# Kernel tuning notes

Measured on AMD Instinct MI355X. Metric: run time of the kernel, lower is better.

The kernel has to match this reference:

```python
import jax, jax.numpy as jnp
import numpy as np

EPS = 1e-6
NUM_GROUPS = 16


def group_norm(x, gamma, beta):
    # x: [B, C, H, W]
    B, C, H, W = x.shape
    xg = x.reshape(B, NUM_GROUPS, C // NUM_GROUPS, H, W)
    mean = xg.mean(axis=(2, 3, 4), keepdims=True)
    var = xg.var(axis=(2, 3, 4), keepdims=True)
    xg = (xg - mean) * jax.lax.rsqrt(var + EPS)
    x = xg.reshape(B, C, H, W)
    return x * gamma[None, :, None, None] + beta[None, :, None, None]


def conv1x1(x, w, b):
    # x: [B, C, H, W], w: [O, C], b: [O]
    return jnp.einsum('bchw,oc->bohw', x, w) + b[None, :, None, None]


def setup_inputs() -> dict:
    key = jax.random.key(0)
    ks = jax.random.split(key, 6)
    B, C, H, W = 8, 256, 64, 64
    s = 1.0 / np.sqrt(C)
    return {
        'x': jax.random.normal(ks[0], (B, C, H, W), dtype=jnp.float32),
        'gamma': jnp.ones((C,), jnp.float32),
        'beta': jnp.zeros((C,), jnp.float32),
        'wq': jax.random.normal(ks[1], (C, C), dtype=jnp.float32) * s,
        'bq': jnp.zeros((C,), jnp.float32),
        'wk': jax.random.normal(ks[2], (C, C), dtype=jnp.float32) * s,
        'bk': jnp.zeros((C,), jnp.float32),
        'wv': jax.random.normal(ks[3], (C, C), dtype=jnp.float32) * s,
        'bv': jnp.zeros((C,), jnp.float32),
        'wp': jax.random.normal(ks[4], (C, C), dtype=jnp.float32) * s,
        'bp': jnp.zeros((C,), jnp.float32),
    }


def reference(x, gamma, beta, wq, bq, wk, bk, wv, bv, wp, bp):
    B, C, H, W = x.shape
    identity = x
    h = group_norm(x, gamma, beta)
    q = conv1x1(h, wq, bq).reshape(B, C, H * W)  # [B, C, N]
    k = conv1x1(h, wk, bk).reshape(B, C, H * W)
    v = conv1x1(h, wv, bv).reshape(B, C, H * W)
    # alpha[b, i, j] = sum_c q[b, c, i] * k[b, c, j], scaled by C^-0.5
    alpha = jnp.einsum('bci,bcj->bij', q, k) * (C ** -0.5)
    alpha = jax.nn.softmax(alpha, axis=-1)
    # out[b, c, i] = sum_j v[b, c, j] * alpha[b, i, j]
    out = jnp.einsum('bcj,bij->bci', v, alpha).reshape(B, C, H, W)
    out = conv1x1(out, wp, bp)
    return identity + out
```

## Files before the change

kernel.cpp:

```cpp
#include <hip/hip_runtime.h>
#include <hip/hip_bf16.h>


typedef unsigned int u32;
typedef unsigned short u16;
typedef __bf16 bf16x8 __attribute__((ext_vector_type(8)));
typedef float f32x4 __attribute__((ext_vector_type(4)));
typedef float f32x16 __attribute__((ext_vector_type(16)));

#define GAS __attribute__((address_space(1)))
#define LAS __attribute__((address_space(3)))

__device__ __forceinline__ u16 f2bf(float f) {
  union { float f; u32 u; } v; v.f = f;
  return (u16)((v.u + 0x7fffu + ((v.u >> 16) & 1u)) >> 16);
}

__device__ __forceinline__ f32x16 mfma32(bf16x8 a, bf16x8 b, f32x16 c) {
  return __builtin_amdgcn_mfma_f32_32x32x16_bf16(a, b, c, 0, 0, 0);
}

template<int ITERS, int NT>
__device__ __forceinline__ void stage_lin(u16* lds, const u16* g, int tid) {
#pragma unroll
  for (int it = 0; it < ITERS; ++it) {
    int idx = it * NT + tid;
    const u16* src = g + (long)idx * 8;
    u16* dst = lds + (long)(idx & ~63) * 8;
    __builtin_amdgcn_global_load_lds((const GAS u32*)src, (LAS u32*)dst, 16, 0, 0);
  }
}

template<int ROWS, int NT>
__device__ __forceinline__ void stage_gran(u16* lds, const u16* g, int k0, int tid) {
  constexpr int ITERS = 4 * ROWS / NT;
#pragma unroll
  for (int it = 0; it < ITERS; ++it) {
    int gi = it * NT + tid;
    int row = gi & (ROWS - 1);
    int kh = gi / ROWS;
    const u16* src = g + (long)row * 256 + k0 + kh * 8;
    u16* dst = lds + (long)(gi & ~63) * 8;
    __builtin_amdgcn_global_load_lds((const GAS u32*)src, (LAS u32*)dst, 16, 0, 0);
  }
}

__global__ __launch_bounds__(256) void convert_w(
    const float* __restrict__ w0, const float* __restrict__ w1,
    const float* __restrict__ w2, const float* __restrict__ w3,
    u16* __restrict__ out) {
  int i = blockIdx.x * 256 + threadIdx.x;
  int seg = i >> 16, idx = i & 65535;
  const float* w = seg == 0 ? w0 : seg == 1 ? w1 : seg == 2 ? w2 : w3;
  out[i] = f2bf(w[idx]);
}

__global__ __launch_bounds__(256) void gn_kernel(
    const float* __restrict__ x, const float* __restrict__ gamma,
    const float* __restrict__ beta, u16* __restrict__ ht) {
  int tid = threadIdx.x;
  int b = blockIdx.x >> 4;
  int grp = blockIdx.x & 15;
  const float* xg = x + ((long)b * 256 + grp * 16) * 4096;

  float s = 0.f, ss = 0.f;
  const float4* x4 = (const float4*)xg;
#pragma unroll 4
  for (int it = 0; it < 64; ++it) {
    float4 v = x4[it * 256 + tid];
    s += v.x + v.y + v.z + v.w;
    ss += v.x * v.x + v.y * v.y + v.z * v.z + v.w * v.w;
  }
#pragma unroll
  for (int d = 1; d < 64; d <<= 1) {
    s += __shfl_xor(s, d);
    ss += __shfl_xor(ss, d);
  }
  __shared__ float red[10];
  int lane = tid & 63, wave = tid >> 6;
  if (lane == 0) { red[wave] = s; red[4 + wave] = ss; }
  __syncthreads();
  if (tid == 0) {
    float S = red[0] + red[1] + red[2] + red[3];
    float SS = red[4] + red[5] + red[6] + red[7];
    float mean = S * (1.f / 65536.f);
    float var = SS * (1.f / 65536.f) - mean * mean;
    red[8] = mean;
    red[9] = rsqrtf(var + 1e-6f);
  }
  __syncthreads();
  float mean = red[8], rstd = red[9];

  float a[16], bb[16];
#pragma unroll
  for (int c = 0; c < 16; ++c) {
    float gm = gamma[grp * 16 + c];
    float bt = beta[grp * 16 + c];
    a[c] = gm * rstd;
    bb[c] = bt - mean * a[c];
  }
  u16* hb = ht + (long)b * 4096 * 256 + grp * 16;
  for (int it = 0; it < 16; ++it) {
    int n = it * 256 + tid;
    __align__(16) u16 tmp[16];
#pragma unroll
    for (int c = 0; c < 16; ++c)
      tmp[c] = f2bf(xg[(long)c * 4096 + n] * a[c] + bb[c]);
    u16* dst = hb + (long)n * 256;
    ((uint4*)dst)[0] = ((uint4*)tmp)[0];
    ((uint4*)dst)[1] = ((uint4*)tmp)[1];
  }
}

__global__ __launch_bounds__(256, 2) void gemm_qkv(
    const u16* __restrict__ ht, const u16* __restrict__ wbf,
    u16* __restrict__ qtb, u16* __restrict__ ktb, u16* __restrict__ vcb,
    const float* __restrict__ bq, const float* __restrict__ bk,
    const float* __restrict__ bv) {
  __shared__ __align__(16) u16 as2[4 * 128 * 8];
  __shared__ __align__(16) u16 bs2[3][4 * 128 * 8];

  int tid = threadIdx.x;
  int lane = tid & 63;
  int h = lane >> 5, lr = lane & 31;
  int wave = tid >> 6;
  int wp = wave >> 1, wo = wave & 1;
  long mrow = (long)blockIdx.x * 128;
  int ob = blockIdx.y * 128;

  f32x16 zero16 = {0,0,0,0,0,0,0,0,0,0,0,0,0,0,0,0};
  f32x16 acc[3][2][2];
#pragma unroll
  for (int m = 0; m < 3; ++m)
#pragma unroll
    for (int p = 0; p < 2; ++p)
#pragma unroll
      for (int q = 0; q < 2; ++q) acc[m][p][q] = zero16;

  const u16* Ab = ht + mrow * 256;

  for (int step = 0; step < 8; ++step) {
    int k0 = step * 32;
    __syncthreads();
    stage_gran<128, 256>(as2, Ab, k0, tid);
    stage_gran<128, 256>(bs2[0], wbf + (long)ob * 256, k0, tid);
    stage_gran<128, 256>(bs2[1], wbf + 65536 + (long)ob * 256, k0, tid);
    stage_gran<128, 256>(bs2[2], wbf + 131072 + (long)ob * 256, k0, tid);
    __syncthreads();

#pragma unroll
    for (int ks = 0; ks < 2; ++ks) {
      int kg = (2 * ks + h) * 128;
      bf16x8 a0 = *(const bf16x8*)(as2 + (long)(kg + wp * 64 + lr) * 8);
      bf16x8 a1 = *(const bf16x8*)(as2 + (long)(kg + wp * 64 + 32 + lr) * 8);
      __builtin_amdgcn_s_setprio(1);
#pragma unroll
      for (int m = 0; m < 3; ++m) {
        bf16x8 b0 = *(const bf16x8*)(bs2[m] + (long)(kg + wo * 64 + lr) * 8);
        bf16x8 b1 = *(const bf16x8*)(bs2[m] + (long)(kg + wo * 64 + 32 + lr) * 8);
        acc[m][0][0] = mfma32(a0, b0, acc[m][0][0]);
        acc[m][0][1] = mfma32(a0, b1, acc[m][0][1]);
        acc[m][1][0] = mfma32(a1, b0, acc[m][1][0]);
        acc[m][1][1] = mfma32(a1, b1, acc[m][1][1]);
      }
      __builtin_amdgcn_s_setprio(0);
    }
  }

  const float QSC = 0.0625f * 1.44269504f;
  long b_ = mrow >> 12;
  int posb = (int)(mrow & 4095);
#pragma unroll
  for (int p = 0; p < 2; ++p)
#pragma unroll
    for (int q = 0; q < 2; ++q) {
      int o = ob + wo * 64 + q * 32 + lr;
      float bqv = bq[o], bkv = bk[o], bvv = bv[o];
      int posl0 = posb + wp * 64 + p * 32;
      int jt = posl0 >> 5;
      long tbase = b_ * 1048576 + (long)jt * 8192;
      long kbase = tbase + (o >> 3) * 256 + (o & 7);
      long vbase = tbase + (long)o * 8;
      long qrow0 = (mrow + wp * 64 + p * 32) * 256 + o;
#pragma unroll
      for (int quad = 0; quad < 4; ++quad) {
        __align__(8) u16 v4[4];
#pragma unroll
        for (int e = 0; e < 4; ++e) {
          int rloc = 8 * quad + 4 * h + e;
          float vq = acc[0][p][q][4 * quad + e];
          float vk = acc[1][p][q][4 * quad + e];
          float vv = acc[2][p][q][4 * quad + e];
          qtb[qrow0 + (long)rloc * 256] = f2bf((vq + bqv) * QSC);
          ktb[kbase + rloc * 8] = f2bf(vk + bkv);
          v4[e] = f2bf(vv + bvv);
        }
        int r0 = 8 * quad + 4 * h;
        *(uint2*)(vcb + vbase + ((r0 >> 3) & 3) * 2048 + (r0 & 7)) = *(uint2*)v4;
      }
    }
}

__global__ __launch_bounds__(256) void gemm_proj(
    const u16* __restrict__ Wp, const u16* __restrict__ ao,
    float* __restrict__ outp, const float* __restrict__ bias,
    const float* __restrict__ resid) {
  __shared__ __align__(16) u16 ws2[4 * 256 * 8];
  __shared__ __align__(16) u16 aos[4 * 64 * 8];

  int tid = threadIdx.x;
  int lane = tid & 63;
  int h = lane >> 5, lr = lane & 31;
  int wo = tid >> 6;
  long b = blockIdx.x & 7;
  int pos0 = (blockIdx.x >> 3) * 64;
  const u16* aob = ao + (b * 4096 + pos0) * 256;

  f32x16 zero16 = {0,0,0,0,0,0,0,0,0,0,0,0,0,0,0,0};
  f32x16 acc[2][2];
#pragma unroll
  for (int p = 0; p < 2; ++p)
#pragma unroll
    for (int q = 0; q < 2; ++q) acc[p][q] = zero16;

  for (int step = 0; step < 8; ++step) {
    int k0 = step * 32;
    __syncthreads();
    stage_gran<256, 256>(ws2, Wp, k0, tid);
    stage_gran<64, 256>(aos, aob, k0, tid);
    __syncthreads();

#pragma unroll
    for (int ks = 0; ks < 2; ++ks) {
      int kgw = (2 * ks + h) * 256;
      int kga = (2 * ks + h) * 64;
      bf16x8 w0 = *(const bf16x8*)(ws2 + (long)(kgw + wo * 64 + lr) * 8);
      bf16x8 w1 = *(const bf16x8*)(ws2 + (long)(kgw + wo * 64 + 32 + lr) * 8);
      bf16x8 o0 = *(const bf16x8*)(aos + (long)(kga + lr) * 8);
      bf16x8 o1 = *(const bf16x8*)(aos + (long)(kga + 32 + lr) * 8);
      __builtin_amdgcn_s_setprio(1);
      acc[0][0] = mfma32(w0, o0, acc[0][0]);
      acc[0][1] = mfma32(w0, o1, acc[0][1]);
      acc[1][0] = mfma32(w1, o0, acc[1][0]);
      acc[1][1] = mfma32(w1, o1, acc[1][1]);
      __builtin_amdgcn_s_setprio(0);
    }
  }

#pragma unroll
  for (int p = 0; p < 2; ++p)
#pragma unroll
    for (int q = 0; q < 2; ++q) {
      int pos = pos0 + q * 32 + lr;
#pragma unroll
      for (int quad = 0; quad < 4; ++quad)
#pragma unroll
        for (int e = 0; e < 4; ++e) {
          int o = wo * 64 + p * 32 + 8 * quad + 4 * h + e;
          long addr = b * 1048576 + (long)o * 4096 + pos;
          outp[addr] = acc[p][q][4 * quad + e] + bias[o] + resid[addr];
        }
    }
}

__global__ __launch_bounds__(128, 2) void attn_flash(
    const u16* __restrict__ qt, const u16* __restrict__ kgp,
    const u16* __restrict__ vgp, u16* __restrict__ part0, u16* __restrict__ part1,
    float2* __restrict__ ml0, float2* __restrict__ ml1) {
  __shared__ __align__(16) u16 ksT[8192];
  __shared__ __align__(16) u16 vsT[8192];
  __shared__ float fws[64];

  int tid = threadIdx.x;
  int lane = tid & 63;
  int h = lane >> 5, lr = lane & 31;
  int rg = tid >> 6;
  int bid = blockIdx.x;
  long b = bid & 7;
  int jhalf = (bid >> 3) & 1;
  int i0 = (bid >> 4) * 64;

  const u16* kb = kgp + b * 1048576 + (long)(jhalf * 64) * 8192;
  const u16* vb = vgp + b * 1048576 + (long)(jhalf * 64) * 8192;
  float* fw = fws + rg * 32;

  const u16* qrow = qt + ((b * 4096 + i0 + rg * 32 + lr) << 8) + h * 8;
  bf16x8 qreg[16];
#pragma unroll
  for (int kk = 0; kk < 16; ++kk)
    qreg[kk] = *(const bf16x8*)(qrow + kk * 16);

  f32x16 zero16 = {0,0,0,0,0,0,0,0,0,0,0,0,0,0,0,0};
  f32x16 acc[8];
#pragma unroll
  for (int ct = 0; ct < 8; ++ct) acc[ct] = zero16;
  float mrun = -3e38f, lsum = 0.f;

  for (int t = 0; t < 64; ++t) {
    __syncthreads();
    stage_lin<8, 128>(ksT, kb + (long)t * 8192, tid);
    stage_lin<8, 128>(vsT, vb + (long)t * 8192, tid);
    __syncthreads();

    f32x16 sacc = zero16;
    __builtin_amdgcn_s_setprio(1);
#pragma unroll
    for (int kk = 0; kk < 16; ++kk) {
      bf16x8 kf = *(const bf16x8*)(ksT + ((2 * kk + h) * 32 + lr) * 8);
      sacc = mfma32(kf, qreg[kk], sacc);
    }
    __builtin_amdgcn_s_setprio(0);

    float m0 = fmaxf(fmaxf(sacc[0], sacc[1]), fmaxf(sacc[2], sacc[3]));
    float m1 = fmaxf(fmaxf(sacc[4], sacc[5]), fmaxf(sacc[6], sacc[7]));
    float m2 = fmaxf(fmaxf(sacc[8], sacc[9]), fmaxf(sacc[10], sacc[11]));
    float m3 = fmaxf(fmaxf(sacc[12], sacc[13]), fmaxf(sacc[14], sacc[15]));
    float mloc = fmaxf(fmaxf(m0, m1), fmaxf(m2, m3));
    mloc = fmaxf(mloc, __shfl_xor(mloc, 32));

    if (!__all(mloc - mrun <= 8.f)) {
      float mnew = fmaxf(mrun, mloc);
      float al = exp2f(mrun - mnew);
      mrun = mnew;
      lsum *= al;
      if (h == 0) fw[lr] = al;
      asm volatile("s_waitcnt lgkmcnt(0)" ::: "memory");
      f32x4 fq0 = *(const f32x4*)&fw[4 * h];
      f32x4 fq1 = *(const f32x4*)&fw[8 + 4 * h];
      f32x4 fq2 = *(const f32x4*)&fw[16 + 4 * h];
      f32x4 fq3 = *(const f32x4*)&fw[24 + 4 * h];
      f32x16 alv;
#pragma unroll
      for (int e = 0; e < 4; ++e) {
        alv[e] = fq0[e]; alv[4 + e] = fq1[e]; alv[8 + e] = fq2[e]; alv[12 + e] = fq3[e];
      }
#pragma unroll
      for (int ct = 0; ct < 8; ++ct) acc[ct] *= alv;
    }

    u32 u[8];
#pragma unroll
    for (int m = 0; m < 8; ++m) {
      float p0 = exp2f(sacc[2 * m] - mrun);
      float p1 = exp2f(sacc[2 * m + 1] - mrun);
      lsum += p0 + p1;
      asm volatile("v_cvt_pk_bf16_f32 %0, %1, %2" : "=v"(u[m]) : "v"(p0), "v"(p1));
    }
    u32 rv[4];
#pragma unroll
    for (int kt2 = 0; kt2 < 2; ++kt2)
#pragma unroll
      for (int idx = 0; idx < 2; ++idx) {
        u32 send = h ? u[4 * kt2 + idx] : u[4 * kt2 + 2 + idx];
        rv[kt2 * 2 + idx] = (u32)__shfl_xor((int)send, 32);
      }
    union { u32 wd[4]; bf16x8 v; } pf[2];
#pragma unroll
    for (int kt2 = 0; kt2 < 2; ++kt2) {
      pf[kt2].wd[0] = h ? rv[kt2 * 2] : u[4 * kt2];
      pf[kt2].wd[1] = h ? rv[kt2 * 2 + 1] : u[4 * kt2 + 1];
      pf[kt2].wd[2] = h ? u[4 * kt2 + 2] : rv[kt2 * 2];
      pf[kt2].wd[3] = h ? u[4 * kt2 + 3] : rv[kt2 * 2 + 1];
    }

    __builtin_amdgcn_s_setprio(1);
#pragma unroll
    for (int ct = 0; ct < 8; ++ct) {
      int c = ct * 32 + lr;
      bf16x8 vf0 = *(const bf16x8*)(vsT + ((long)h * 256 + c) * 8);
      bf16x8 vf1 = *(const bf16x8*)(vsT + ((long)(2 + h) * 256 + c) * 8);
      acc[ct] = mfma32(pf[0].v, vf0, acc[ct]);
      acc[ct] = mfma32(pf[1].v, vf1, acc[ct]);
    }
    __builtin_amdgcn_s_setprio(0);
  }

  lsum += __shfl_xor(lsum, 32);
  u16* pout = jhalf ? part1 : part0;
  float2* mlo = jhalf ? ml1 : ml0;
  if (h == 0)
    mlo[b * 4096 + i0 + rg * 32 + lr] = make_float2(mrun, lsum);
  u16* ob = pout + ((b * 4096 + i0 + rg * 32) << 8);
#pragma unroll
  for (int ct = 0; ct < 8; ++ct) {
    int c = ct * 32 + lr;
#pragma unroll
    for (int q = 0; q < 4; ++q)
#pragma unroll
      for (int e = 0; e < 4; ++e) {
        int i = 8 * q + 4 * h + e;
        ob[(long)i * 256 + c] = f2bf(acc[ct][4 * q + e]);
      }
  }
}

__global__ __launch_bounds__(256) void attn_merge(
    const u16* __restrict__ p0, const u16* __restrict__ p1,
    const float2* __restrict__ ml0, const float2* __restrict__ ml1,
    u16* __restrict__ out) {
  int tid = threadIdx.x;
  int row = blockIdx.x * 16 + (tid >> 4);
  int cs = (tid & 15) * 16;
  float2 a = ml0[row], c = ml1[row];
  float M = fmaxf(a.x, c.x);
  float w0 = exp2f(a.x - M), w1 = exp2f(c.x - M);
  float rl = 1.0f / (w0 * a.y + w1 * c.y);
  float f0 = w0 * rl, f1 = w1 * rl;

  long base = (long)row * 256 + cs;
  bf16x8 a0 = *(const bf16x8*)(p0 + base);
  bf16x8 a1 = *(const bf16x8*)(p0 + base + 8);
  bf16x8 c0 = *(const bf16x8*)(p1 + base);
  bf16x8 c1 = *(const bf16x8*)(p1 + base + 8);
  __align__(16) u16 o[16];
#pragma unroll
  for (int k = 0; k < 8; ++k) {
    o[k]     = f2bf(f0 * (float)a0[k] + f1 * (float)c0[k]);
    o[k + 8] = f2bf(f0 * (float)a1[k] + f1 * (float)c1[k]);
  }
  *(uint4*)(out + base) = ((uint4*)o)[0];
  *(uint4*)(out + base + 8) = ((uint4*)o)[1];
}

extern "C" void kernel_launch(void* const* d_in, const int* in_sizes, int n_in,
                              void* d_out, int out_size, void* d_ws, size_t ws_size,
                              hipStream_t stream) {
  const float* x     = (const float*)d_in[0];
  const float* gamma = (const float*)d_in[1];
  const float* beta  = (const float*)d_in[2];
  const float* wq = (const float*)d_in[3];
  const float* bq = (const float*)d_in[4];
  const float* wk = (const float*)d_in[5];
  const float* bk = (const float*)d_in[6];
  const float* wv = (const float*)d_in[7];
  const float* bv = (const float*)d_in[8];
  const float* wp = (const float*)d_in[9];
  const float* bp = (const float*)d_in[10];

  char* ws = (char*)d_ws;
  const long SZ = 16777216;
  u16* ht  = (u16*)(ws);
  u16* qtb = (u16*)(ws + SZ);
  u16* ktb = (u16*)(ws + 2 * SZ);
  u16* vcb = (u16*)(ws + 3 * SZ);
  u16* wbf = (u16*)(ws + 4 * SZ);
  u16* part0 = ht;
  u16* part1 = (u16*)d_out;
  float2* ml0 = (float2*)((char*)d_out + SZ);
  float2* ml1 = (float2*)((char*)d_out + SZ + 262144);

  convert_w<<<1024, 256, 0, stream>>>(wq, wk, wv, wp, wbf);
  gn_kernel<<<128, 256, 0, stream>>>(x, gamma, beta, ht);

  dim3 gq(256, 2, 1);
  gemm_qkv<<<gq, 256, 0, stream>>>(ht, wbf, qtb, ktb, vcb, bq, bk, bv);

  attn_flash<<<1024, 128, 0, stream>>>(qtb, ktb, vcb, part0, part1, ml0, ml1);

  attn_merge<<<2048, 256, 0, stream>>>(part0, part1, ml0, ml1, qtb);

  dim3 gp(512, 1, 1);
  gemm_proj<<<gp, 256, 0, stream>>>(wbf + 3 * 65536, qtb, (float*)d_out, bp, x);
}
```

Before: 333.8 us.

## Double-buffer K/V tiles in flash attention with 256-thread blocks

The flash attention kernel now uses 256-thread blocks covering 128 query rows, sharing each K/V tile across four waves instead of two. K/V tiles are double-buffered in LDS, and the next tile's global loads are issued before computing on the current one, with a partial vmcnt wait and raw barriers. The goal is to hide global-load latency behind the MFMA work and halve K/V staging traffic per query row. In exchange LDS use per block doubles, which may reduce occupancy. The hand-tuned vmcnt count also depends on exactly how many loads stage_lin issues per call.

```diff
diff --git a/kernel.cpp b/kernel.cpp
--- a/kernel.cpp
+++ b/kernel.cpp
@@ -263,13 +263,13 @@
     }
 }
 
-__global__ __launch_bounds__(128, 2) void attn_flash(
+__global__ __launch_bounds__(256, 2) void attn_flash(
     const u16* __restrict__ qt, const u16* __restrict__ kgp,
     const u16* __restrict__ vgp, u16* __restrict__ part0, u16* __restrict__ part1,
     float2* __restrict__ ml0, float2* __restrict__ ml1) {
-  __shared__ __align__(16) u16 ksT[8192];
-  __shared__ __align__(16) u16 vsT[8192];
-  __shared__ float fws[64];
+  __shared__ __align__(16) u16 ksT[2 * 8192];
+  __shared__ __align__(16) u16 vsT[2 * 8192];
+  __shared__ float fws[128];
 
   int tid = threadIdx.x;
   int lane = tid & 63;
@@ -278,7 +278,7 @@
   int bid = blockIdx.x;
   long b = bid & 7;
   int jhalf = (bid >> 3) & 1;
-  int i0 = (bid >> 4) * 64;
+  int i0 = (bid >> 4) * 128;
 
   const u16* kb = kgp + b * 1048576 + (long)(jhalf * 64) * 8192;
   const u16* vb = vgp + b * 1048576 + (long)(jhalf * 64) * 8192;
@@ -296,17 +296,31 @@
   for (int ct = 0; ct < 8; ++ct) acc[ct] = zero16;
   float mrun = -3e38f, lsum = 0.f;
 
+  stage_lin<4, 256>(ksT, kb, tid);
+  stage_lin<4, 256>(vsT, vb, tid);
+
   for (int t = 0; t < 64; ++t) {
-    __syncthreads();
-    stage_lin<8, 128>(ksT, kb + (long)t * 8192, tid);
-    stage_lin<8, 128>(vsT, vb + (long)t * 8192, tid);
-    __syncthreads();
+    int cur = t & 1, nxt = cur ^ 1;
+    __builtin_amdgcn_s_barrier();
+    __builtin_amdgcn_sched_barrier(0);
+    if (t < 63) {
+      stage_lin<4, 256>(ksT + nxt * 8192, kb + (long)(t + 1) * 8192, tid);
+      stage_lin<4, 256>(vsT + nxt * 8192, vb + (long)(t + 1) * 8192, tid);
+    }
+    __builtin_amdgcn_sched_barrier(0);
+    asm volatile("s_waitcnt vmcnt(8)" ::: "memory");
+    __builtin_amdgcn_sched_barrier(0);
+    __builtin_amdgcn_s_barrier();
+    __builtin_amdgcn_sched_barrier(0);
+
+    const u16* ksl = ksT + cur * 8192;
+    const u16* vsl = vsT + cur * 8192;
 
     f32x16 sacc = zero16;
     __builtin_amdgcn_s_setprio(1);
 #pragma unroll
     for (int kk = 0; kk < 16; ++kk) {
-      bf16x8 kf = *(const bf16x8*)(ksT + ((2 * kk + h) * 32 + lr) * 8);
+      bf16x8 kf = *(const bf16x8*)(ksl + ((2 * kk + h) * 32 + lr) * 8);
       sacc = mfma32(kf, qreg[kk], sacc);
     }
     __builtin_amdgcn_s_setprio(0);
@@ -367,12 +381,13 @@
 #pragma unroll
     for (int ct = 0; ct < 8; ++ct) {
       int c = ct * 32 + lr;
-      bf16x8 vf0 = *(const bf16x8*)(vsT + ((long)h * 256 + c) * 8);
-      bf16x8 vf1 = *(const bf16x8*)(vsT + ((long)(2 + h) * 256 + c) * 8);
+      bf16x8 vf0 = *(const bf16x8*)(vsl + ((long)h * 256 + c) * 8);
+      bf16x8 vf1 = *(const bf16x8*)(vsl + ((long)(2 + h) * 256 + c) * 8);
       acc[ct] = mfma32(pf[0].v, vf0, acc[ct]);
       acc[ct] = mfma32(pf[1].v, vf1, acc[ct]);
     }
     __builtin_amdgcn_s_setprio(0);
+    __builtin_amdgcn_sched_barrier(0);
   }
 
   lsum += __shfl_xor(lsum, 32);
@@ -455,7 +470,7 @@
   dim3 gq(256, 2, 1);
   gemm_qkv<<<gq, 256, 0, stream>>>(ht, wbf, qtb, ktb, vcb, bq, bk, bv);
 
-  attn_flash<<<1024, 128, 0, stream>>>(qtb, ktb, vcb, part0, part1, ml0, ml1);
+  attn_flash<<<512, 256, 0, stream>>>(qtb, ktb, vcb, part0, part1, ml0, ml1);
 
   attn_merge<<<2048, 256, 0, stream>>>(part0, part1, ml0, ml1, qtb);
 
```

New measurement: 312.2 us. 1.07x faster.
